# Optimization experiments

Measured on AMD Instinct MI355X. Metric: run time of the kernel, lower is better.

The kernel has to match this reference:

```python
import jax, jax.numpy as jnp
import numpy as np

N = 100000
E = 1_600_000
IN_DIM = 128
HIDDEN = 128


def spmm(row, col, vals, H):
    # y[r] = sum_{edges e with row[e]==r} vals[e] * H[col[e]]
    msgs = vals[:, None] * H[col]          # [E, hidden] gather + scale
    return jax.ops.segment_sum(msgs, row, num_segments=H.shape[0])


def setup_inputs() -> dict:
    key = jax.random.key(0)
    ks = jax.random.split(key, 10)
    X = jax.random.normal(ks[0], (N, IN_DIM), dtype=jnp.float32)
    row = jax.random.randint(ks[1], (E,), 0, N, dtype=jnp.int32)
    col = jax.random.randint(ks[2], (E,), 0, N, dtype=jnp.int32)
    vals = jax.random.uniform(ks[3], (E,), dtype=jnp.float32)
    s_in = 1.0 / np.sqrt(IN_DIM)
    s_h = 1.0 / np.sqrt(HIDDEN)
    W_in = jax.random.normal(ks[4], (IN_DIM, HIDDEN), dtype=jnp.float32) * s_in
    b_in = jax.random.normal(ks[5], (HIDDEN,), dtype=jnp.float32) * s_in
    W_mp1 = jax.random.normal(ks[6], (HIDDEN, HIDDEN), dtype=jnp.float32) * s_h
    W_mp2 = jax.random.normal(ks[7], (HIDDEN, HIDDEN), dtype=jnp.float32) * s_h
    W_out = jax.random.normal(ks[8], (HIDDEN, 1), dtype=jnp.float32) * s_h
    b_out = jax.random.normal(ks[9], (1,), dtype=jnp.float32) * s_h
    return {"X": X, "row": row, "col": col, "vals": vals,
            "W_in": W_in, "b_in": b_in, "W_mp1": W_mp1, "W_mp2": W_mp2,
            "W_out": W_out, "b_out": b_out}


def reference(X, row, col, vals, W_in, b_in, W_mp1, W_mp2, W_out, b_out):
    H = jax.nn.relu(X @ W_in + b_in)          # [N, hidden]
    AH = spmm(row, col, vals, H)              # 1-hop propagation
    A2H = spmm(row, col, vals, AH)            # 2-hop propagation
    H2 = jax.nn.relu(AH @ W_mp1 + A2H @ W_mp2)
    return H2 @ W_out + b_out                 # [N, 1]
```

## Files before the change

kernel.cpp:

```cpp
#include <hip/hip_runtime.h>

#define N_NODES 100000
#define N_EDGES 1600000
#define NBUCK 391
#define NCHUNK 256
#define CHUNK 6250
#define LROW 136
#define DCAP 5120
#define GSPLIT 782

typedef float f32x4 __attribute__((ext_vector_type(4)));
typedef _Float16 f16x8 __attribute__((ext_vector_type(8)));
typedef _Float16 h16x2 __attribute__((ext_vector_type(2)));

__device__ __forceinline__ unsigned f2h_bits(float f) {
    union { _Float16 h; unsigned short s; } c;
    c.h = (_Float16)f;
    return c.s;
}
__device__ __forceinline__ h16x2 u2h(unsigned u) {
    union { unsigned u; h16x2 h; } c;
    c.u = u;
    return c.h;
}
__device__ __forceinline__ unsigned pk16lo(unsigned hi, unsigned lo) {
    return __builtin_amdgcn_perm(hi, lo, 0x05040100u);
}
__device__ __forceinline__ unsigned pk16hi(unsigned hi, unsigned lo) {
    return __builtin_amdgcn_perm(hi, lo, 0x07060302u);
}
__device__ __forceinline__ float fdot2(h16x2 a, h16x2 b, float c) {
#if __has_builtin(__builtin_amdgcn_fdot2)
    return __builtin_amdgcn_fdot2(a, b, c, false);
#else
    return c + (float)a[0] * (float)b[0] + (float)a[1] * (float)b[1];
#endif
}

__device__ __forceinline__ f16x8 pack_h8(float4 a, float4 b) {
    f16x8 r;
    r[0] = (_Float16)a.x; r[1] = (_Float16)a.y;
    r[2] = (_Float16)a.z; r[3] = (_Float16)a.w;
    r[4] = (_Float16)b.x; r[5] = (_Float16)b.y;
    r[6] = (_Float16)b.z; r[7] = (_Float16)b.w;
    return r;
}

__device__ __forceinline__ void gemm_in_tile(int tilebase,
                                             const float* __restrict__ X,
                                             const unsigned short* __restrict__ Wt,
                                             const float* __restrict__ bvec,
                                             unsigned short* __restrict__ H,
                                             unsigned short* lds) {
    int tid = threadIdx.x;
    int lane = tid & 63, wv = tid >> 6;
    int quad = lane >> 4, c16 = lane & 15;

    f16x8 wf[2][4];
    float bb[2];
#pragma unroll
    for (int nt = 0; nt < 2; nt++) {
        int ng = wv * 2 + nt;
        bb[nt] = bvec[ng * 16 + c16];
#pragma unroll
        for (int kc = 0; kc < 4; kc++)
            wf[nt][kc] = *(const f16x8*)&Wt[(ng * 16 + c16) * 128 + kc * 32 + quad * 8];
    }

    const float4* Xg = (const float4*)X;
#pragma unroll
    for (int i = 0; i < 4; i++) {
        int c = tid + i * 256;
        int r = c >> 4, o = c & 15;
        int grow = tilebase + r;
        float4 f0 = make_float4(0.f, 0.f, 0.f, 0.f), f1 = f0;
        if (grow < N_NODES) {
            f0 = Xg[(size_t)grow * 32 + o * 2];
            f1 = Xg[(size_t)grow * 32 + o * 2 + 1];
        }
        *(f16x8*)&lds[r * LROW + o * 8] = pack_h8(f0, f1);
    }
    __syncthreads();

    f32x4 acc[4][2] = {};
#pragma unroll
    for (int t4 = 0; t4 < 4; t4++) {
#pragma unroll
        for (int kc = 0; kc < 4; kc++) {
            f16x8 af = *(const f16x8*)&lds[(t4 * 16 + c16) * LROW + kc * 32 + quad * 8];
#pragma unroll
            for (int nt = 0; nt < 2; nt++)
                acc[t4][nt] = __builtin_amdgcn_mfma_f32_16x16x32_f16(af, wf[nt][kc],
                                                                    acc[t4][nt], 0, 0, 0);
        }
    }
    __syncthreads();

#pragma unroll
    for (int t4 = 0; t4 < 4; t4++)
#pragma unroll
        for (int nt = 0; nt < 2; nt++) {
            int ncol = (wv * 2 + nt) * 16 + c16;
#pragma unroll
            for (int r = 0; r < 4; r++) {
                float v = fmaxf(acc[t4][nt][r] + bb[nt], 0.f);
                lds[(t4 * 16 + quad * 4 + r) * LROW + ncol] = (unsigned short)f2h_bits(v);
            }
        }
    __syncthreads();
#pragma unroll
    for (int i = 0; i < 4; i++) {
        int c = tid + i * 256;
        int r = c >> 4, o = c & 15;
        int grow = tilebase + r;
        if (grow < N_NODES)
            *(uint4*)&H[(size_t)grow * 128 + o * 8] = *(const uint4*)&lds[r * LROW + o * 8];
    }
}


__global__ __launch_bounds__(512) void k_prep(const int* __restrict__ row,
                                              int* __restrict__ hmat,
                                              const float* __restrict__ Wa,
                                              const float* __restrict__ Wb,
                                              const float* __restrict__ Wc,
                                              unsigned short* __restrict__ Wta,
                                              unsigned short* __restrict__ Wtb,
                                              unsigned short* __restrict__ Wtc) {
    if (blockIdx.x < NCHUNK) {
        __shared__ int h[NBUCK];
        for (int i = threadIdx.x; i < NBUCK; i += 512) h[i] = 0;
        __syncthreads();
        int s = blockIdx.x * CHUNK, e = s + CHUNK;
        for (int i = s + threadIdx.x; i < e; i += 512)
            atomicAdd(&h[row[i] >> 8], 1);
        __syncthreads();
        for (int b = threadIdx.x; b < NBUCK; b += 512)
            hmat[blockIdx.x * NBUCK + b] = h[b];
    } else {
        int t = (blockIdx.x - NCHUNK) * 512 + threadIdx.x;
        int which = t >> 14;
        int i = t & 16383;
        int n = i & 127, k = i >> 7;
        const float* W = which == 0 ? Wa : which == 1 ? Wb : Wc;
        unsigned short* Wt = which == 0 ? Wta : which == 1 ? Wtb : Wtc;
        Wt[n * 128 + k] = (unsigned short)f2h_bits(W[k * 128 + n]);
    }
}

__global__ __launch_bounds__(512) void k_colscanB(const int* __restrict__ hmat,
                                                  int* __restrict__ bases,
                                                  int* __restrict__ bstart) {
    __shared__ int s[512];
    int b = blockIdx.x, t = threadIdx.x;
    if (b < NBUCK) {
        int v = (t < NCHUNK) ? hmat[t * NBUCK + b] : 0;
        s[t] = v;
        __syncthreads();
        for (int off = 1; off < 512; off <<= 1) {
            int x = (t >= off) ? s[t - off] : 0;
            __syncthreads();
            s[t] += x;
            __syncthreads();
        }
        if (t < NCHUNK) bases[t * NBUCK + b] = s[t] - v;
    } else {
        int v = 0;
        if (t < NBUCK) {
            for (int blk = 0; blk < NCHUNK; blk++) v += hmat[blk * NBUCK + t];
        }
        s[t] = v;
        __syncthreads();
        for (int off = 1; off < 512; off <<= 1) {
            int x = (t >= off) ? s[t - off] : 0;
            __syncthreads();
            s[t] += x;
            __syncthreads();
        }
        if (t < NBUCK) bstart[t] = s[t] - v;
        if (t == NBUCK) bstart[NBUCK] = N_EDGES;
    }
}

__global__ __launch_bounds__(256) void k_binC_gemmA(const int* __restrict__ row,
                                                    const int* __restrict__ col,
                                                    const float* __restrict__ vals,
                                                    const int* __restrict__ bstart,
                                                    const int* __restrict__ bases,
                                                    int2* __restrict__ grouped,
                                                    const float* __restrict__ X,
                                                    const unsigned short* __restrict__ Wt,
                                                    const float* __restrict__ bvec,
                                                    unsigned short* __restrict__ H) {
    __shared__ __align__(16) char smraw[64 * LROW * 2];
    if (blockIdx.x < NCHUNK) {
        int* cnt = (int*)smraw;
        int* basl = (int*)(smraw + 1600);
        for (int i = threadIdx.x; i < NBUCK; i += 256) {
            cnt[i] = 0;
            basl[i] = bstart[i] + bases[blockIdx.x * NBUCK + i];
        }
        __syncthreads();
        int s = blockIdx.x * CHUNK, e = s + CHUNK;
        for (int i = s + threadIdx.x; i < e; i += 256) {
            int r = row[i];
            int b = r >> 8;
            int rank = atomicAdd(&cnt[b], 1);
            int pos = basl[b] + rank;
            unsigned hv = f2h_bits(vals[i]);
            grouped[pos] = make_int2(col[i], ((r & 255) << 14) | hv);
        }
    } else {
        gemm_in_tile((blockIdx.x - NCHUNK) * 64, X, Wt, bvec, H,
                     (unsigned short*)smraw);
    }
}

__global__ __launch_bounds__(256) void k_binD_gemmB(const int2* __restrict__ grouped,
                                                    const int* __restrict__ bstart,
                                                    unsigned* __restrict__ evf,
                                                    int* __restrict__ row_ptr,
                                                    const float* __restrict__ X,
                                                    const unsigned short* __restrict__ Wt,
                                                    const float* __restrict__ bvec,
                                                    unsigned short* __restrict__ H) {
    __shared__ __align__(16) char smraw[DCAP * 8 + 3 * 256 * 4];
    if (blockIdx.x < NBUCK) {
        int* h = (int*)smraw;
        int* sc = h + 256;
        int* cur = sc + 256;
        int2* ebuf = (int2*)(smraw + 3 * 256 * 4);
        int b = blockIdx.x, t = threadIdx.x;
        int s0 = bstart[b], e0 = bstart[b + 1];
        int n = e0 - s0;
        bool inlds = (n <= DCAP);
        h[t] = 0;
        __syncthreads();
        if (inlds) {
            for (int i = t; i < n; i += 256) ebuf[i] = grouped[s0 + i];
            __syncthreads();
            for (int i = t; i < n; i += 256)
                atomicAdd(&h[(ebuf[i].y >> 14) & 255], 1);
        } else {
            for (int i = s0 + t; i < e0; i += 256)
                atomicAdd(&h[(grouped[i].y >> 14) & 255], 1);
        }
        __syncthreads();
        int v = h[t];
        sc[t] = v;
        __syncthreads();
        for (int off = 1; off < 256; off <<= 1) {
            int x = (t >= off) ? sc[t - off] : 0;
            __syncthreads();
            sc[t] += x;
            __syncthreads();
        }
        int excl = sc[t] - v;
        cur[t] = excl;
        int grow = b * 256 + t;
        if (grow <= N_NODES) row_ptr[grow] = s0 + excl;
        __syncthreads();
        if (inlds) {
            for (int i = t; i < n; i += 256) {
                int2 g = ebuf[i];
                int rl = (g.y >> 14) & 255;
                int p = atomicAdd(&cur[rl], 1);
                evf[s0 + p] = ((unsigned)g.x << 14) | (unsigned)(g.y & 0x3fff);
            }
        } else {
            for (int i = s0 + t; i < e0; i += 256) {
                int2 g = grouped[i];
                int rl = (g.y >> 14) & 255;
                int p = atomicAdd(&cur[rl], 1);
                evf[s0 + p] = ((unsigned)g.x << 14) | (unsigned)(g.y & 0x3fff);
            }
        }
    } else {
        gemm_in_tile((GSPLIT + (int)blockIdx.x - NBUCK) * 64, X, Wt, bvec, H,
                     (unsigned short*)smraw);
    }
}

__global__ __launch_bounds__(256) void k_spmm(const int* __restrict__ rp,
                                              const unsigned* __restrict__ evf,
                                              const unsigned* __restrict__ Hin,
                                              unsigned* __restrict__ Ho) {
    int wid = (blockIdx.x * blockDim.x + threadIdx.x) >> 6;
    int lane = threadIdx.x & 63;
    if (wid >= N_NODES) return;
    int q = lane >> 4, l16 = lane & 15;
    int s = __builtin_amdgcn_readfirstlane(rp[wid]);
    int e = __builtin_amdgcn_readfirstlane(rp[wid + 1]);
    float a0 = 0.f, a1 = 0.f, a2 = 0.f, a3 = 0.f;
    float a4 = 0.f, a5 = 0.f, a6 = 0.f, a7 = 0.f;
    for (int base = s; base < e; base += 64) {
        int cnt = e - base;
        if (cnt > 64) cnt = 64;
        unsigned ev = evf[base + (lane < cnt ? lane : cnt - 1)];
        int r = 0;
        for (; r + 16 <= cnt; r += 16) {
            unsigned u0 = __shfl(ev, r + q, 64);
            unsigned u1 = __shfl(ev, r + 4 + q, 64);
            unsigned u2 = __shfl(ev, r + 8 + q, 64);
            unsigned u3 = __shfl(ev, r + 12 + q, 64);
            const uint4 h0 = *(const uint4*)&Hin[(size_t)(u0 >> 14) * 64 + l16 * 4];
            const uint4 h1 = *(const uint4*)&Hin[(size_t)(u1 >> 14) * 64 + l16 * 4];
            const uint4 h2 = *(const uint4*)&Hin[(size_t)(u2 >> 14) * 64 + l16 * 4];
            const uint4 h3 = *(const uint4*)&Hin[(size_t)(u3 >> 14) * 64 + l16 * 4];
            h16x2 v01 = u2h(pk16lo(u1 & 0x3fffu, u0 & 0x3fffu));
            h16x2 v23 = u2h(pk16lo(u3 & 0x3fffu, u2 & 0x3fffu));
            a0 = fdot2(v01, u2h(pk16lo(h1.x, h0.x)), a0);
            a0 = fdot2(v23, u2h(pk16lo(h3.x, h2.x)), a0);
            a1 = fdot2(v01, u2h(pk16hi(h1.x, h0.x)), a1);
            a1 = fdot2(v23, u2h(pk16hi(h3.x, h2.x)), a1);
            a2 = fdot2(v01, u2h(pk16lo(h1.y, h0.y)), a2);
            a2 = fdot2(v23, u2h(pk16lo(h3.y, h2.y)), a2);
            a3 = fdot2(v01, u2h(pk16hi(h1.y, h0.y)), a3);
            a3 = fdot2(v23, u2h(pk16hi(h3.y, h2.y)), a3);
            a4 = fdot2(v01, u2h(pk16lo(h1.z, h0.z)), a4);
            a4 = fdot2(v23, u2h(pk16lo(h3.z, h2.z)), a4);
            a5 = fdot2(v01, u2h(pk16hi(h1.z, h0.z)), a5);
            a5 = fdot2(v23, u2h(pk16hi(h3.z, h2.z)), a5);
            a6 = fdot2(v01, u2h(pk16lo(h1.w, h0.w)), a6);
            a6 = fdot2(v23, u2h(pk16lo(h3.w, h2.w)), a6);
            a7 = fdot2(v01, u2h(pk16hi(h1.w, h0.w)), a7);
            a7 = fdot2(v23, u2h(pk16hi(h3.w, h2.w)), a7);
        }
        if (r < cnt) {
            int i0 = r + q, i1 = r + 4 + q, i2 = r + 8 + q, i3 = r + 12 + q;
            unsigned u0 = __shfl(ev, i0 < cnt ? i0 : cnt - 1, 64);
            unsigned u1 = __shfl(ev, i1 < cnt ? i1 : cnt - 1, 64);
            unsigned u2 = __shfl(ev, i2 < cnt ? i2 : cnt - 1, 64);
            unsigned u3 = __shfl(ev, i3 < cnt ? i3 : cnt - 1, 64);
            const uint4 h0 = *(const uint4*)&Hin[(size_t)(u0 >> 14) * 64 + l16 * 4];
            const uint4 h1 = *(const uint4*)&Hin[(size_t)(u1 >> 14) * 64 + l16 * 4];
            const uint4 h2 = *(const uint4*)&Hin[(size_t)(u2 >> 14) * 64 + l16 * 4];
            const uint4 h3 = *(const uint4*)&Hin[(size_t)(u3 >> 14) * 64 + l16 * 4];
            unsigned m0 = (i0 < cnt) ? (u0 & 0x3fffu) : 0u;
            unsigned m1 = (i1 < cnt) ? (u1 & 0x3fffu) : 0u;
            unsigned m2 = (i2 < cnt) ? (u2 & 0x3fffu) : 0u;
            unsigned m3 = (i3 < cnt) ? (u3 & 0x3fffu) : 0u;
            h16x2 v01 = u2h(pk16lo(m1, m0));
            h16x2 v23 = u2h(pk16lo(m3, m2));
            a0 = fdot2(v01, u2h(pk16lo(h1.x, h0.x)), a0);
            a0 = fdot2(v23, u2h(pk16lo(h3.x, h2.x)), a0);
            a1 = fdot2(v01, u2h(pk16hi(h1.x, h0.x)), a1);
            a1 = fdot2(v23, u2h(pk16hi(h3.x, h2.x)), a1);
            a2 = fdot2(v01, u2h(pk16lo(h1.y, h0.y)), a2);
            a2 = fdot2(v23, u2h(pk16lo(h3.y, h2.y)), a2);
            a3 = fdot2(v01, u2h(pk16hi(h1.y, h0.y)), a3);
            a3 = fdot2(v23, u2h(pk16hi(h3.y, h2.y)), a3);
            a4 = fdot2(v01, u2h(pk16lo(h1.z, h0.z)), a4);
            a4 = fdot2(v23, u2h(pk16lo(h3.z, h2.z)), a4);
            a5 = fdot2(v01, u2h(pk16hi(h1.z, h0.z)), a5);
            a5 = fdot2(v23, u2h(pk16hi(h3.z, h2.z)), a5);
            a6 = fdot2(v01, u2h(pk16lo(h1.w, h0.w)), a6);
            a6 = fdot2(v23, u2h(pk16lo(h3.w, h2.w)), a6);
            a7 = fdot2(v01, u2h(pk16hi(h1.w, h0.w)), a7);
            a7 = fdot2(v23, u2h(pk16hi(h3.w, h2.w)), a7);
        }
    }
    a0 += __shfl_xor(a0, 16, 64); a0 += __shfl_xor(a0, 32, 64);
    a1 += __shfl_xor(a1, 16, 64); a1 += __shfl_xor(a1, 32, 64);
    a2 += __shfl_xor(a2, 16, 64); a2 += __shfl_xor(a2, 32, 64);
    a3 += __shfl_xor(a3, 16, 64); a3 += __shfl_xor(a3, 32, 64);
    a4 += __shfl_xor(a4, 16, 64); a4 += __shfl_xor(a4, 32, 64);
    a5 += __shfl_xor(a5, 16, 64); a5 += __shfl_xor(a5, 32, 64);
    a6 += __shfl_xor(a6, 16, 64); a6 += __shfl_xor(a6, 32, 64);
    a7 += __shfl_xor(a7, 16, 64); a7 += __shfl_xor(a7, 32, 64);
    if (q == 0) {
        uint4 p;
        p.x = (f2h_bits(a1) << 16) | f2h_bits(a0);
        p.y = (f2h_bits(a3) << 16) | f2h_bits(a2);
        p.z = (f2h_bits(a5) << 16) | f2h_bits(a4);
        p.w = (f2h_bits(a7) << 16) | f2h_bits(a6);
        *(uint4*)&Ho[(size_t)wid * 64 + l16 * 4] = p;
    }
}

__global__ __launch_bounds__(256) void k_gemm_out(const unsigned short* __restrict__ AH,
                                                  const unsigned short* __restrict__ A2H,
                                                  const unsigned short* __restrict__ Wt1,
                                                  const unsigned short* __restrict__ Wt2,
                                                  const float* __restrict__ Wout,
                                                  const float* __restrict__ bout,
                                                  float* __restrict__ out) {
    __shared__ unsigned short lds[2][64 * LROW];
    __shared__ float part[4][64];
    int tid = threadIdx.x;
    int lane = tid & 63, wv = tid >> 6;
    int quad = lane >> 4, c16 = lane & 15;

    f16x8 w1f[2][4], w2f[2][4];
    float wo[2];
#pragma unroll
    for (int nt = 0; nt < 2; nt++) {
        int ng = wv * 2 + nt;
        wo[nt] = Wout[ng * 16 + c16];
#pragma unroll
        for (int kc = 0; kc < 4; kc++) {
            w1f[nt][kc] = *(const f16x8*)&Wt1[(ng * 16 + c16) * 128 + kc * 32 + quad * 8];
            w2f[nt][kc] = *(const f16x8*)&Wt2[(ng * 16 + c16) * 128 + kc * 32 + quad * 8];
        }
    }
    float bo = bout[0];

    int tilebase = blockIdx.x * 64;
    const uint4* Ag = (const uint4*)(AH + (size_t)tilebase * 128);
    const uint4* Bg = (const uint4*)(A2H + (size_t)tilebase * 128);
#pragma unroll
    for (int i = 0; i < 4; i++) {
        int c = tid + i * 256;
        int r = c >> 4, o = c & 15;
        *(uint4*)&lds[0][r * LROW + o * 8] = Ag[c];
        *(uint4*)&lds[1][r * LROW + o * 8] = Bg[c];
    }
    __syncthreads();

    f32x4 acc[4][2] = {};
#pragma unroll
    for (int t4 = 0; t4 < 4; t4++) {
#pragma unroll
        for (int kc = 0; kc < 4; kc++) {
            f16x8 afA = *(const f16x8*)&lds[0][(t4 * 16 + c16) * LROW + kc * 32 + quad * 8];
            f16x8 afB = *(const f16x8*)&lds[1][(t4 * 16 + c16) * LROW + kc * 32 + quad * 8];
#pragma unroll
            for (int nt = 0; nt < 2; nt++) {
                acc[t4][nt] = __builtin_amdgcn_mfma_f32_16x16x32_f16(afA, w1f[nt][kc],
                                                                    acc[t4][nt], 0, 0, 0);
                acc[t4][nt] = __builtin_amdgcn_mfma_f32_16x16x32_f16(afB, w2f[nt][kc],
                                                                    acc[t4][nt], 0, 0, 0);
            }
        }
    }

#pragma unroll
    for (int t4 = 0; t4 < 4; t4++) {
        float p[4];
#pragma unroll
        for (int r = 0; r < 4; r++)
            p[r] = fmaxf(acc[t4][0][r], 0.f) * wo[0] + fmaxf(acc[t4][1][r], 0.f) * wo[1];
#pragma unroll
        for (int m = 1; m < 16; m <<= 1)
#pragma unroll
            for (int r = 0; r < 4; r++) p[r] += __shfl_xor(p[r], m, 64);
        if (c16 == 0)
#pragma unroll
            for (int r = 0; r < 4; r++) part[wv][t4 * 16 + quad * 4 + r] = p[r];
    }
    __syncthreads();
    if (tid < 64) {
        int orow = tilebase + tid;
        if (orow < N_NODES)
            out[orow] = part[0][tid] + part[1][tid] + part[2][tid] + part[3][tid] + bo;
    }
}


extern "C" void kernel_launch(void* const* d_in, const int* in_sizes, int n_in,
                              void* d_out, int out_size, void* d_ws, size_t ws_size,
                              hipStream_t stream) {
    const float* X    = (const float*)d_in[0];
    const int*   row  = (const int*)d_in[1];
    const int*   col  = (const int*)d_in[2];
    const float* vals = (const float*)d_in[3];
    const float* W_in = (const float*)d_in[4];
    const float* b_in = (const float*)d_in[5];
    const float* W1   = (const float*)d_in[6];
    const float* W2   = (const float*)d_in[7];
    const float* Wout = (const float*)d_in[8];
    const float* bout = (const float*)d_in[9];
    float* out = (float*)d_out;

    char* ws = (char*)d_ws;
    size_t off = 0;
    auto alloc = [&](size_t bytes) -> void* {
        void* p = ws + off;
        off += (bytes + 511) & ~(size_t)511;
        return p;
    };
    unsigned short* Hb  = (unsigned short*)alloc((size_t)N_NODES * 128 * 2);
    unsigned short* AHb = (unsigned short*)alloc((size_t)N_NODES * 128 * 2);
    unsigned short* A2b = (unsigned short*)alloc((size_t)N_NODES * 128 * 2);
    unsigned* evf  = (unsigned*)alloc((size_t)N_EDGES * 4);
    int2* grouped  = (int2*)alloc((size_t)N_EDGES * 8);
    unsigned short* Wtin = (unsigned short*)alloc(128 * 128 * 2);
    unsigned short* Wt1  = (unsigned short*)alloc(128 * 128 * 2);
    unsigned short* Wt2  = (unsigned short*)alloc(128 * 128 * 2);
    int*   hmat    = (int*)alloc((size_t)NCHUNK * NBUCK * 4);
    int*   bases   = (int*)alloc((size_t)NCHUNK * NBUCK * 4);
    int*   bstart  = (int*)alloc(512 * 4);
    int*   row_ptr = (int*)alloc((size_t)(N_NODES + 256) * 4);

    int gblk = (N_NODES + 63) / 64;

    k_prep<<<NCHUNK + 96, 512, 0, stream>>>(row, hmat, W_in, W1, W2, Wtin, Wt1, Wt2);
    k_colscanB<<<NBUCK + 1, 512, 0, stream>>>(hmat, bases, bstart);
    k_binC_gemmA<<<NCHUNK + GSPLIT, 256, 0, stream>>>(row, col, vals, bstart, bases,
                                                      grouped, X, Wtin, b_in, Hb);
    k_binD_gemmB<<<NBUCK + (gblk - GSPLIT), 256, 0, stream>>>(grouped, bstart, evf,
                                                              row_ptr, X, Wtin, b_in, Hb);

    int sblk = (N_NODES + 3) / 4;
    k_spmm<<<sblk, 256, 0, stream>>>(row_ptr, evf, (const unsigned*)Hb, (unsigned*)AHb);
    k_spmm<<<sblk, 256, 0, stream>>>(row_ptr, evf, (const unsigned*)AHb, (unsigned*)A2b);

    k_gemm_out<<<gblk, 256, 0, stream>>>(AHb, A2b, Wt1, Wt2, Wout, bout, out);
}
```

Before: 301.8 us.

## Replace histogram-and-scan binning with global atomic cursors into fixed-capacity buckets

Removes the separate per-chunk histogram kernel and the column-scan kernel. Each binning block now counts its own bucket sizes in shared memory and reserves space with one global atomicAdd per bucket into fixed slots of CAP entries. The second binning stage recovers each bucket's start offset by reducing the counts of the preceding buckets. This saves two launches and the extra scan pass, but `row` is read twice inside the binning block. Correctness depends on no bucket exceeding CAP edges, which nothing checks. Edge order within a bucket also becomes nondeterministic.

```diff
diff --git a/kernel.cpp b/kernel.cpp
--- a/kernel.cpp
+++ b/kernel.cpp
@@ -7,6 +7,7 @@
 #define CHUNK 6250
 #define LROW 136
 #define DCAP 5120
+#define CAP 5120
 #define GSPLIT 782
 
 typedef float f32x4 __attribute__((ext_vector_type(4)));
@@ -119,74 +120,30 @@
 }
 
 
-__global__ __launch_bounds__(512) void k_prep(const int* __restrict__ row,
-                                              int* __restrict__ hmat,
-                                              const float* __restrict__ Wa,
+__global__ __launch_bounds__(512) void k_init(const float* __restrict__ Wa,
                                               const float* __restrict__ Wb,
                                               const float* __restrict__ Wc,
                                               unsigned short* __restrict__ Wta,
                                               unsigned short* __restrict__ Wtb,
-                                              unsigned short* __restrict__ Wtc) {
-    if (blockIdx.x < NCHUNK) {
-        __shared__ int h[NBUCK];
-        for (int i = threadIdx.x; i < NBUCK; i += 512) h[i] = 0;
-        __syncthreads();
-        int s = blockIdx.x * CHUNK, e = s + CHUNK;
-        for (int i = s + threadIdx.x; i < e; i += 512)
-            atomicAdd(&h[row[i] >> 8], 1);
-        __syncthreads();
-        for (int b = threadIdx.x; b < NBUCK; b += 512)
-            hmat[blockIdx.x * NBUCK + b] = h[b];
-    } else {
-        int t = (blockIdx.x - NCHUNK) * 512 + threadIdx.x;
+                                              unsigned short* __restrict__ Wtc,
+                                              int* __restrict__ gcur) {
+    if (blockIdx.x < 96) {
+        int t = blockIdx.x * 512 + threadIdx.x;
         int which = t >> 14;
         int i = t & 16383;
         int n = i & 127, k = i >> 7;
         const float* W = which == 0 ? Wa : which == 1 ? Wb : Wc;
         unsigned short* Wt = which == 0 ? Wta : which == 1 ? Wtb : Wtc;
         Wt[n * 128 + k] = (unsigned short)f2h_bits(W[k * 128 + n]);
-    }
-}
-
-__global__ __launch_bounds__(512) void k_colscanB(const int* __restrict__ hmat,
-                                                  int* __restrict__ bases,
-                                                  int* __restrict__ bstart) {
-    __shared__ int s[512];
-    int b = blockIdx.x, t = threadIdx.x;
-    if (b < NBUCK) {
-        int v = (t < NCHUNK) ? hmat[t * NBUCK + b] : 0;
-        s[t] = v;
-        __syncthreads();
-        for (int off = 1; off < 512; off <<= 1) {
-            int x = (t >= off) ? s[t - off] : 0;
-            __syncthreads();
-            s[t] += x;
-            __syncthreads();
-        }
-        if (t < NCHUNK) bases[t * NBUCK + b] = s[t] - v;
     } else {
-        int v = 0;
-        if (t < NBUCK) {
-            for (int blk = 0; blk < NCHUNK; blk++) v += hmat[blk * NBUCK + t];
-        }
-        s[t] = v;
-        __syncthreads();
-        for (int off = 1; off < 512; off <<= 1) {
-            int x = (t >= off) ? s[t - off] : 0;
-            __syncthreads();
-            s[t] += x;
-            __syncthreads();
-        }
-        if (t < NBUCK) bstart[t] = s[t] - v;
-        if (t == NBUCK) bstart[NBUCK] = N_EDGES;
+        gcur[threadIdx.x] = 0;
     }
 }
 
 __global__ __launch_bounds__(256) void k_binC_gemmA(const int* __restrict__ row,
                                                     const int* __restrict__ col,
                                                     const float* __restrict__ vals,
-                                                    const int* __restrict__ bstart,
-                                                    const int* __restrict__ bases,
+                                                    int* __restrict__ gcur,
                                                     int2* __restrict__ grouped,
                                                     const float* __restrict__ X,
                                                     const unsigned short* __restrict__ Wt,
@@ -195,18 +152,25 @@
     __shared__ __align__(16) char smraw[64 * LROW * 2];
     if (blockIdx.x < NCHUNK) {
         int* cnt = (int*)smraw;
-        int* basl = (int*)(smraw + 1600);
-        for (int i = threadIdx.x; i < NBUCK; i += 256) {
-            cnt[i] = 0;
-            basl[i] = bstart[i] + bases[blockIdx.x * NBUCK + i];
-        }
+        int* basg = cnt + NBUCK;
+        int* rnk = basg + NBUCK;
+        int t = threadIdx.x;
+        for (int i = t; i < NBUCK; i += 256) { cnt[i] = 0; rnk[i] = 0; }
         __syncthreads();
         int s = blockIdx.x * CHUNK, e = s + CHUNK;
-        for (int i = s + threadIdx.x; i < e; i += 256) {
+        for (int i = s + t; i < e; i += 256)
+            atomicAdd(&cnt[row[i] >> 8], 1);
+        __syncthreads();
+        for (int b = t; b < NBUCK; b += 256) {
+            int c = cnt[b];
+            basg[b] = c ? atomicAdd(&gcur[b], c) : 0;
+        }
+        __syncthreads();
+        for (int i = s + t; i < e; i += 256) {
             int r = row[i];
             int b = r >> 8;
-            int rank = atomicAdd(&cnt[b], 1);
-            int pos = basl[b] + rank;
+            int rank = atomicAdd(&rnk[b], 1);
+            int pos = b * CAP + basg[b] + rank;
             unsigned hv = f2h_bits(vals[i]);
             grouped[pos] = make_int2(col[i], ((r & 255) << 14) | hv);
         }
@@ -217,7 +181,7 @@
 }
 
 __global__ __launch_bounds__(256) void k_binD_gemmB(const int2* __restrict__ grouped,
-                                                    const int* __restrict__ bstart,
+                                                    const int* __restrict__ gcur,
                                                     unsigned* __restrict__ evf,
                                                     int* __restrict__ row_ptr,
                                                     const float* __restrict__ X,
@@ -231,19 +195,28 @@
         int* cur = sc + 256;
         int2* ebuf = (int2*)(smraw + 3 * 256 * 4);
         int b = blockIdx.x, t = threadIdx.x;
-        int s0 = bstart[b], e0 = bstart[b + 1];
-        int n = e0 - s0;
+        int part = 0;
+        for (int j = t; j < b; j += 256) part += gcur[j];
+        sc[t] = part;
+        __syncthreads();
+        for (int off = 128; off > 0; off >>= 1) {
+            if (t < off) sc[t] += sc[t + off];
+            __syncthreads();
+        }
+        int s0 = sc[0];
+        int n = gcur[b];
+        const int2* src = grouped + (size_t)b * CAP;
         bool inlds = (n <= DCAP);
         h[t] = 0;
         __syncthreads();
         if (inlds) {
-            for (int i = t; i < n; i += 256) ebuf[i] = grouped[s0 + i];
+            for (int i = t; i < n; i += 256) ebuf[i] = src[i];
             __syncthreads();
             for (int i = t; i < n; i += 256)
                 atomicAdd(&h[(ebuf[i].y >> 14) & 255], 1);
         } else {
-            for (int i = s0 + t; i < e0; i += 256)
-                atomicAdd(&h[(grouped[i].y >> 14) & 255], 1);
+            for (int i = t; i < n; i += 256)
+                atomicAdd(&h[(src[i].y >> 14) & 255], 1);
         }
         __syncthreads();
         int v = h[t];
@@ -268,8 +241,8 @@
                 evf[s0 + p] = ((unsigned)g.x << 14) | (unsigned)(g.y & 0x3fff);
             }
         } else {
-            for (int i = s0 + t; i < e0; i += 256) {
-                int2 g = grouped[i];
+            for (int i = t; i < n; i += 256) {
+                int2 g = src[i];
                 int rl = (g.y >> 14) & 255;
                 int p = atomicAdd(&cur[rl], 1);
                 evf[s0 + p] = ((unsigned)g.x << 14) | (unsigned)(g.y & 0x3fff);
@@ -483,22 +456,19 @@
     unsigned short* AHb = (unsigned short*)alloc((size_t)N_NODES * 128 * 2);
     unsigned short* A2b = (unsigned short*)alloc((size_t)N_NODES * 128 * 2);
     unsigned* evf  = (unsigned*)alloc((size_t)N_EDGES * 4);
-    int2* grouped  = (int2*)alloc((size_t)N_EDGES * 8);
+    int2* grouped  = (int2*)alloc((size_t)NBUCK * CAP * 8);
     unsigned short* Wtin = (unsigned short*)alloc(128 * 128 * 2);
     unsigned short* Wt1  = (unsigned short*)alloc(128 * 128 * 2);
     unsigned short* Wt2  = (unsigned short*)alloc(128 * 128 * 2);
-    int*   hmat    = (int*)alloc((size_t)NCHUNK * NBUCK * 4);
-    int*   bases   = (int*)alloc((size_t)NCHUNK * NBUCK * 4);
-    int*   bstart  = (int*)alloc(512 * 4);
+    int*   gcur    = (int*)alloc(512 * 4);
     int*   row_ptr = (int*)alloc((size_t)(N_NODES + 256) * 4);
 
     int gblk = (N_NODES + 63) / 64;
 
-    k_prep<<<NCHUNK + 96, 512, 0, stream>>>(row, hmat, W_in, W1, W2, Wtin, Wt1, Wt2);
-    k_colscanB<<<NBUCK + 1, 512, 0, stream>>>(hmat, bases, bstart);
-    k_binC_gemmA<<<NCHUNK + GSPLIT, 256, 0, stream>>>(row, col, vals, bstart, bases,
+    k_init<<<97, 512, 0, stream>>>(W_in, W1, W2, Wtin, Wt1, Wt2, gcur);
+    k_binC_gemmA<<<NCHUNK + GSPLIT, 256, 0, stream>>>(row, col, vals, gcur,
                                                       grouped, X, Wtin, b_in, Hb);
-    k_binD_gemmB<<<NBUCK + (gblk - GSPLIT), 256, 0, stream>>>(grouped, bstart, evf,
+    k_binD_gemmB<<<NBUCK + (gblk - GSPLIT), 256, 0, stream>>>(grouped, gcur, evf,
                                                               row_ptr, X, Wtin, b_in, Hb);
 
     int sblk = (N_NODES + 3) / 4;
```

After: 298.2 us. About the same (-1.2%).
